# Optimization experiments

Hardware: AMD Instinct MI355X
Metric: run time of the kernel (lower is better)

The kernel has to match this reference:

```python
import jax, jax.numpy as jnp
import numpy as np

TGT, SRC, BH, D = 2048, 2048, 16, 64

def setup_inputs() -> dict:
    key = jax.random.key(0)
    kq, kk, kv, km = jax.random.split(key, 4)
    return {
        "query": jax.random.normal(kq, (TGT, BH, D), dtype=jnp.float32),
        "key": jax.random.normal(kk, (SRC, BH, D), dtype=jnp.float32),
        "value": jax.random.normal(kv, (SRC, BH, D), dtype=jnp.float32),
        "attn_mask": jax.random.randint(km, (1, TGT, SRC), 0, 2).astype(jnp.bool_),
    }

def reference(query, key, value, attn_mask):
    # seq-first layout: [len, batch_heads, head_dim] -> [bh, len, d]
    head_dim = query.shape[-1]
    q = jnp.swapaxes(query, 0, 1) * (float(head_dim) ** -0.5)  # [bh, tgt, d]
    k = jnp.swapaxes(key, 0, 1)                                # [bh, src, d]
    v = jnp.swapaxes(value, 0, 1)                              # [bh, src, d]
    w = jnp.einsum('btd,bsd->bts', q, k)                       # [bh, tgt, src]
    w = jnp.where(attn_mask, jnp.float32(-1e8), w)
    w = jax.nn.softmax(w, axis=-1)
    # dropout p=0.0 (eval) -> identity
    out = jnp.einsum('bts,bsd->btd', w, v)                     # [bh, tgt, d]
    return jnp.swapaxes(out, 0, 1), w  # ([tgt, bh, d], [bh, tgt, src])
```

## Files before the change

kernel.cpp:

```cpp
#include <hip/hip_runtime.h>

#define TGT 2048
#define SRC 2048
#define BH 16
#define HD 64
#define BT 16
#define SROW 2056

typedef __bf16 bf16x8 __attribute__((ext_vector_type(8)));
typedef unsigned short ushortx8 __attribute__((ext_vector_type(8)));
typedef float floatx4 __attribute__((ext_vector_type(4)));

__device__ int g_mask_is_u8;

__device__ __forceinline__ unsigned short f2bf(float f) {
  unsigned u = __builtin_bit_cast(unsigned, f);
  u += 0x7FFFu + ((u >> 16) & 1u);
  return (unsigned short)(u >> 16);
}
__device__ __forceinline__ float bf2f(unsigned short s) {
  unsigned u = ((unsigned)s) << 16;
  return __builtin_bit_cast(float, u);
}

__global__ void detect_mask_fmt(const unsigned char* __restrict__ m) {
  __shared__ int any;
  if (threadIdx.x == 0) any = 0;
  __syncthreads();
  int local = 0;
  int base = threadIdx.x * 16;
#pragma unroll
  for (int i = 0; i < 16; ++i) {
    int idx = base + i;
    if (idx & 3) local |= m[idx];
  }
  if (local) atomicOr(&any, 1);
  __syncthreads();
  if (threadIdx.x == 0) g_mask_is_u8 = (any != 0);
}

__global__ void mask_pack(const unsigned char* __restrict__ m8,
                          const int* __restrict__ m32,
                          unsigned char* __restrict__ bm) {
  const int gid = blockIdx.x * 256 + threadIdx.x;
  const bool is_u8 = (g_mask_is_u8 != 0);
  const size_t base = (size_t)gid * 32;
  unsigned bits = 0;
  if (is_u8) {
    const uint4 a = *(const uint4*)(m8 + base);
    const uint4 b = *(const uint4*)(m8 + base + 16);
    unsigned w[8] = {a.x, a.y, a.z, a.w, b.x, b.y, b.z, b.w};
#pragma unroll
    for (int wi = 0; wi < 8; ++wi)
#pragma unroll
      for (int j = 0; j < 4; ++j)
        if ((w[wi] >> (8 * j)) & 0xFFu) bits |= 1u << (wi * 4 + j);
  } else {
#pragma unroll
    for (int c = 0; c < 8; ++c) {
      const int4 a = *(const int4*)(m32 + base + c * 4);
      if (a.x) bits |= 1u << (c * 4 + 0);
      if (a.y) bits |= 1u << (c * 4 + 1);
      if (a.z) bits |= 1u << (c * 4 + 2);
      if (a.w) bits |= 1u << (c * 4 + 3);
    }
  }
  *(unsigned*)(bm + (size_t)gid * 4) = bits;
}

__global__ void cvt_qk(const float* __restrict__ q, const float* __restrict__ k,
                       unsigned short* __restrict__ qb, unsigned short* __restrict__ kb) {
  const int gid = blockIdx.x * 256 + threadIdx.x;
  const int half = TGT * BH * HD / 8;
  const float* src; unsigned short* dst; float sc;
  int idx;
  if (gid < half) { src = q; dst = qb; sc = 0.125f; idx = gid; }
  else            { src = k; dst = kb; sc = 1.0f;  idx = gid - half; }
  const float* p = src + (size_t)idx * 8;
  float4 a = *(const float4*)p;
  float4 b = *(const float4*)(p + 4);
  union { unsigned short u[8]; ushortx8 v; } o;
  o.u[0] = f2bf(a.x * sc); o.u[1] = f2bf(a.y * sc);
  o.u[2] = f2bf(a.z * sc); o.u[3] = f2bf(a.w * sc);
  o.u[4] = f2bf(b.x * sc); o.u[5] = f2bf(b.y * sc);
  o.u[6] = f2bf(b.z * sc); o.u[7] = f2bf(b.w * sc);
  *(ushortx8*)(dst + (size_t)idx * 8) = o.v;
}

__global__ void v_tr(const float* __restrict__ v, unsigned short* __restrict__ vt) {
  __shared__ unsigned short tile[64 * 72];
  const int h = blockIdx.x >> 5;
  const int s0 = (blockIdx.x & 31) * 64;
  const int tid = threadIdx.x;
  const int sr = tid >> 4, c = tid & 15;
#pragma unroll
  for (int p = 0; p < 4; ++p) {
    const int s = sr + p * 16;
    float4 f = *(const float4*)(v + (size_t)(s0 + s) * (BH * HD) + h * HD + c * 4);
    tile[(c * 4 + 0) * 72 + s] = f2bf(f.x);
    tile[(c * 4 + 1) * 72 + s] = f2bf(f.y);
    tile[(c * 4 + 2) * 72 + s] = f2bf(f.z);
    tile[(c * 4 + 3) * 72 + s] = f2bf(f.w);
  }
  __syncthreads();
  const int d = tid >> 2, q4 = tid & 3;
  ushortx8 o0 = *(const ushortx8*)&tile[d * 72 + q4 * 16];
  ushortx8 o1 = *(const ushortx8*)&tile[d * 72 + q4 * 16 + 8];
  unsigned short* dst = vt + (size_t)h * HD * SRC + (size_t)d * SRC + s0 + q4 * 16;
  *(ushortx8*)dst = o0;
  *(ushortx8*)(dst + 8) = o1;
}

__launch_bounds__(1024, 8)
__global__ void attn_kernel(const unsigned short* __restrict__ qb,
                            const unsigned short* __restrict__ kb,
                            const unsigned short* __restrict__ vtb,
                            const unsigned char* __restrict__ bmask,
                            float* __restrict__ out0,
                            float* __restrict__ wout) {
  extern __shared__ char smem[];
  unsigned short* smS = (unsigned short*)smem;
  float* scratch = (float*)(smem + BT * SROW * 2);
  float* maxpart = scratch + 3072;
  float* rowmaxArr = maxpart + 256;
  float* invArr = rowmaxArr + BT;

  const int bid0 = blockIdx.x;
  const int bid = (bid0 & 7) * 256 + (bid0 >> 3);
  const int h = bid >> 7;
  const int t0 = (bid & 127) * BT;
  const int tid = threadIdx.x;
  const int wv = tid >> 6;
  const int lane = tid & 63;
  const int quad = lane >> 4;
  const int l16 = lane & 15;

  {
    const unsigned* bg = (const unsigned*)(bmask + (size_t)t0 * (SRC / 8));
    ((unsigned*)scratch)[tid] = bg[tid];
  }

  bf16x8 aq[2];
  {
    const unsigned short* qp = qb + (size_t)(t0 + l16) * (BH * HD) + h * HD + quad * 8;
    aq[0] = __builtin_bit_cast(bf16x8, *(const ushortx8*)qp);
    aq[1] = __builtin_bit_cast(bf16x8, *(const ushortx8*)(qp + 32));
  }
  __syncthreads();

  const unsigned short* smBits = (const unsigned short*)scratch;
  float pmax[4] = {-3.4e38f, -3.4e38f, -3.4e38f, -3.4e38f};
  for (int st = wv; st < SRC / 16; st += 16) {
    const int sbase = st * 16;
    const unsigned short* kp = kb + (size_t)(sbase + l16) * (BH * HD) + h * HD + quad * 8;
    bf16x8 bk0 = __builtin_bit_cast(bf16x8, *(const ushortx8*)kp);
    bf16x8 bk1 = __builtin_bit_cast(bf16x8, *(const ushortx8*)(kp + 32));
    floatx4 c = {0.f, 0.f, 0.f, 0.f};
    c = __builtin_amdgcn_mfma_f32_16x16x32_bf16(aq[0], bk0, c, 0, 0, 0);
    c = __builtin_amdgcn_mfma_f32_16x16x32_bf16(aq[1], bk1, c, 0, 0, 0);
    const int scol = sbase + l16;
#pragma unroll
    for (int r = 0; r < 4; ++r) {
      const int tl = quad * 4 + r;
      const unsigned bits = smBits[tl * (SRC / 16) + st];
      const float val = ((bits >> l16) & 1u) ? -1e8f : c[r];
      pmax[r] = fmaxf(pmax[r], val);
      const float oth = __shfl_xor(val, 1);
      if (!(l16 & 1)) {
        unsigned pk2 = (unsigned)f2bf(val) | ((unsigned)f2bf(oth) << 16);
        *(unsigned*)&smS[tl * SROW + scol] = pk2;
      }
    }
  }
#pragma unroll
  for (int r = 0; r < 4; ++r) {
    float m = pmax[r];
    m = fmaxf(m, __shfl_xor(m, 1));
    m = fmaxf(m, __shfl_xor(m, 2));
    m = fmaxf(m, __shfl_xor(m, 4));
    m = fmaxf(m, __shfl_xor(m, 8));
    if (l16 == 0) maxpart[(quad * 4 + r) * 16 + wv] = m;
  }
  __syncthreads();
  if (tid < BT) {
    float m = maxpart[tid * 16];
    for (int j = 1; j < 16; ++j) m = fmaxf(m, maxpart[tid * 16 + j]);
    rowmaxArr[tid] = m;
  }
  __syncthreads();

  {
    const int row = tid >> 6;
    const int cc = tid & 63;
    const float rm = rowmaxArr[row];
    unsigned short* srow = smS + row * SROW;
    float psum = 0.f;
#pragma unroll
    for (int kk = 0; kk < 4; ++kk) {
      const int col = cc * 8 + kk * 512;
      ushortx8 u = *(const ushortx8*)&srow[col];
      union { unsigned short u[8]; ushortx8 v; } o;
#pragma unroll
      for (int i = 0; i < 8; ++i) {
        float e = __expf(bf2f(u[i]) - rm);
        psum += e;
        o.u[i] = f2bf(e);
      }
      *(ushortx8*)&srow[col] = o.v;
    }
    scratch[row * 64 + cc] = psum;
  }
  __syncthreads();
  if (tid < BT) {
    float s = 0.f;
    for (int j = 0; j < 64; ++j) s += scratch[tid * 64 + j];
    invArr[tid] = 1.0f / s;
  }
  __syncthreads();

  {
    const int row = tid >> 6;
    const int cc = tid & 63;
    const float invv = invArr[row];
    float* wrow = wout + ((size_t)h * TGT + (t0 + row)) * SRC;
    const unsigned short* srow = smS + row * SROW;
#pragma unroll
    for (int kk = 0; kk < 4; ++kk) {
      const int col = cc * 8 + kk * 512;
      ushortx8 u = *(const ushortx8*)&srow[col];
      float4 a, b;
      a.x = bf2f(u[0]) * invv; a.y = bf2f(u[1]) * invv;
      a.z = bf2f(u[2]) * invv; a.w = bf2f(u[3]) * invv;
      b.x = bf2f(u[4]) * invv; b.y = bf2f(u[5]) * invv;
      b.z = bf2f(u[6]) * invv; b.w = bf2f(u[7]) * invv;
      *(float4*)&wrow[col] = a;
      *(float4*)&wrow[col + 4] = b;
    }
  }

  {
    const int dt = wv & 3;
    const int qr = wv >> 2;
    const int dbase = dt * 16;
    const int sstart = qr * 512;
    const unsigned short* vp = vtb + (size_t)h * HD * SRC +
                               (size_t)(dbase + l16) * SRC + sstart + quad * 8;
    const unsigned short* sp = smS + l16 * SROW + sstart + quad * 8;
    floatx4 acc = {0.f, 0.f, 0.f, 0.f};
    for (int s0 = 0; s0 < 512; s0 += 32) {
      bf16x8 af = __builtin_bit_cast(bf16x8, *(const ushortx8*)(sp + s0));
      bf16x8 bfv = __builtin_bit_cast(bf16x8, *(const ushortx8*)(vp + s0));
      acc = __builtin_amdgcn_mfma_f32_16x16x32_bf16(af, bfv, acc, 0, 0, 0);
    }
    if (qr) {
#pragma unroll
      for (int r = 0; r < 4; ++r)
        scratch[((qr - 1) * 4 + dt) * 256 + (quad * 4 + r) * 16 + l16] = acc[r];
    }
    __syncthreads();
    if (!qr) {
#pragma unroll
      for (int r = 0; r < 4; ++r) {
        const int tl = quad * 4 + r;
        float s = acc[r] + scratch[(0 * 4 + dt) * 256 + tl * 16 + l16]
                         + scratch[(1 * 4 + dt) * 256 + tl * 16 + l16]
                         + scratch[(2 * 4 + dt) * 256 + tl * 16 + l16];
        out0[((size_t)(t0 + tl) * BH + h) * HD + dbase + l16] = s * invArr[tl];
      }
    }
  }
}

extern "C" void kernel_launch(void* const* d_in, const int* in_sizes, int n_in,
                              void* d_out, int out_size, void* d_ws, size_t ws_size,
                              hipStream_t stream) {
  const float* q = (const float*)d_in[0];
  const float* k = (const float*)d_in[1];
  const float* v = (const float*)d_in[2];
  const unsigned char* m8 = (const unsigned char*)d_in[3];
  const int* m32 = (const int*)d_in[3];
  float* out0 = (float*)d_out;
  float* wout = out0 + (size_t)TGT * BH * HD;

  unsigned short* qb = (unsigned short*)d_ws;
  unsigned short* kb = qb + (size_t)TGT * BH * HD;
  unsigned short* vt = kb + (size_t)SRC * BH * HD;
  unsigned char* bmask = (unsigned char*)(vt + (size_t)BH * HD * SRC);

  const size_t shbytes = (size_t)BT * SROW * 2 + 3072 * 4 + 256 * 4 + BT * 4 + BT * 4;
  hipFuncSetAttribute((const void*)attn_kernel,
                      hipFuncAttributeMaxDynamicSharedMemorySize, (int)shbytes);

  detect_mask_fmt<<<1, 256, 0, stream>>>(m8);
  mask_pack<<<dim3(512), dim3(256), 0, stream>>>(m8, m32, bmask);
  cvt_qk<<<dim3(2048), dim3(256), 0, stream>>>(q, k, qb, kb);
  v_tr<<<dim3(BH * (SRC / 64)), dim3(256), 0, stream>>>(v, vt);
  attn_kernel<<<dim3(BH * (TGT / BT)), dim3(1024), shbytes, stream>>>(
      qb, kb, vt, bmask, out0, wout);
}
```

Before: 433.3 us.

## Keep softmax scores in registers and fuse max, exp, normalize and store

The QK^T MFMA operands are swapped so each lane holds a row's scores for a contiguous chunk of columns. Each wave now handles a contiguous 128-column slice and keeps the masked scores in registers. Row max, exp, sum and normalisation run in registers with shuffle-plus-LDS reductions, and the weights are written straight to global memory and to LDS once for the PV MFMA. This removes the repeated LDS round-trips and several barriers of the separate softmax passes. It also pads the mask scratch rows and adds s_setprio around the MFMAs, at the cost of more registers per thread.

```diff
diff --git a/kernel.cpp b/kernel.cpp
--- a/kernel.cpp
+++ b/kernel.cpp
@@ -120,10 +120,11 @@
                             float* __restrict__ wout) {
   extern __shared__ char smem[];
   unsigned short* smS = (unsigned short*)smem;
-  float* scratch = (float*)(smem + BT * SROW * 2);
-  float* maxpart = scratch + 3072;
-  float* rowmaxArr = maxpart + 256;
-  float* invArr = rowmaxArr + BT;
+  float* dscratch = (float*)(smem + BT * SROW * 2);
+  unsigned* scratchM = (unsigned*)dscratch;
+  float* maxpart = dscratch + 1088;
+  float* sumpart = dscratch + 1344;
+  float* invArr = (float*)(smem + BT * SROW * 2 + 12288);
 
   const int bid0 = blockIdx.x;
   const int bid = (bid0 & 7) * 256 + (bid0 >> 3);
@@ -137,7 +138,8 @@
 
   {
     const unsigned* bg = (const unsigned*)(bmask + (size_t)t0 * (SRC / 8));
-    ((unsigned*)scratch)[tid] = bg[tid];
+    const int row = tid >> 6, col = tid & 63;
+    scratchM[row * 68 + col] = bg[row * 64 + col];
   }
 
   bf16x8 aq[2];
@@ -148,95 +150,89 @@
   }
   __syncthreads();
 
-  const unsigned short* smBits = (const unsigned short*)scratch;
-  float pmax[4] = {-3.4e38f, -3.4e38f, -3.4e38f, -3.4e38f};
-  for (int st = wv; st < SRC / 16; st += 16) {
-    const int sbase = st * 16;
+  const uint4 mw = *(const uint4*)&scratchM[l16 * 68 + wv * 4];
+
+  const int sb0 = wv * 128;
+  unsigned pp[16];
+  float pmax = -3.4e38f;
+#pragma unroll
+  for (int j = 0; j < 8; ++j) {
+    const int sbase = sb0 + j * 16;
     const unsigned short* kp = kb + (size_t)(sbase + l16) * (BH * HD) + h * HD + quad * 8;
     bf16x8 bk0 = __builtin_bit_cast(bf16x8, *(const ushortx8*)kp);
     bf16x8 bk1 = __builtin_bit_cast(bf16x8, *(const ushortx8*)(kp + 32));
     floatx4 c = {0.f, 0.f, 0.f, 0.f};
-    c = __builtin_amdgcn_mfma_f32_16x16x32_bf16(aq[0], bk0, c, 0, 0, 0);
-    c = __builtin_amdgcn_mfma_f32_16x16x32_bf16(aq[1], bk1, c, 0, 0, 0);
-    const int scol = sbase + l16;
-#pragma unroll
-    for (int r = 0; r < 4; ++r) {
-      const int tl = quad * 4 + r;
-      const unsigned bits = smBits[tl * (SRC / 16) + st];
-      const float val = ((bits >> l16) & 1u) ? -1e8f : c[r];
-      pmax[r] = fmaxf(pmax[r], val);
-      const float oth = __shfl_xor(val, 1);
-      if (!(l16 & 1)) {
-        unsigned pk2 = (unsigned)f2bf(val) | ((unsigned)f2bf(oth) << 16);
-        *(unsigned*)&smS[tl * SROW + scol] = pk2;
-      }
-    }
-  }
-#pragma unroll
-  for (int r = 0; r < 4; ++r) {
-    float m = pmax[r];
-    m = fmaxf(m, __shfl_xor(m, 1));
-    m = fmaxf(m, __shfl_xor(m, 2));
-    m = fmaxf(m, __shfl_xor(m, 4));
-    m = fmaxf(m, __shfl_xor(m, 8));
-    if (l16 == 0) maxpart[(quad * 4 + r) * 16 + wv] = m;
-  }
-  __syncthreads();
-  if (tid < BT) {
-    float m = maxpart[tid * 16];
-    for (int j = 1; j < 16; ++j) m = fmaxf(m, maxpart[tid * 16 + j]);
-    rowmaxArr[tid] = m;
-  }
-  __syncthreads();
-
-  {
-    const int row = tid >> 6;
-    const int cc = tid & 63;
-    const float rm = rowmaxArr[row];
-    unsigned short* srow = smS + row * SROW;
-    float psum = 0.f;
-#pragma unroll
-    for (int kk = 0; kk < 4; ++kk) {
-      const int col = cc * 8 + kk * 512;
-      ushortx8 u = *(const ushortx8*)&srow[col];
-      union { unsigned short u[8]; ushortx8 v; } o;
-#pragma unroll
-      for (int i = 0; i < 8; ++i) {
-        float e = __expf(bf2f(u[i]) - rm);
-        psum += e;
-        o.u[i] = f2bf(e);
-      }
-      *(ushortx8*)&srow[col] = o.v;
-    }
-    scratch[row * 64 + cc] = psum;
-  }
-  __syncthreads();
-  if (tid < BT) {
-    float s = 0.f;
-    for (int j = 0; j < 64; ++j) s += scratch[tid * 64 + j];
-    invArr[tid] = 1.0f / s;
-  }
-  __syncthreads();
-
-  {
-    const int row = tid >> 6;
-    const int cc = tid & 63;
-    const float invv = invArr[row];
-    float* wrow = wout + ((size_t)h * TGT + (t0 + row)) * SRC;
-    const unsigned short* srow = smS + row * SROW;
-#pragma unroll
-    for (int kk = 0; kk < 4; ++kk) {
-      const int col = cc * 8 + kk * 512;
-      ushortx8 u = *(const ushortx8*)&srow[col];
-      float4 a, b;
-      a.x = bf2f(u[0]) * invv; a.y = bf2f(u[1]) * invv;
-      a.z = bf2f(u[2]) * invv; a.w = bf2f(u[3]) * invv;
-      b.x = bf2f(u[4]) * invv; b.y = bf2f(u[5]) * invv;
-      b.z = bf2f(u[6]) * invv; b.w = bf2f(u[7]) * invv;
-      *(float4*)&wrow[col] = a;
-      *(float4*)&wrow[col + 4] = b;
-    }
-  }
+    __builtin_amdgcn_s_setprio(1);
+    c = __builtin_amdgcn_mfma_f32_16x16x32_bf16(bk0, aq[0], c, 0, 0, 0);
+    c = __builtin_amdgcn_mfma_f32_16x16x32_bf16(bk1, aq[1], c, 0, 0, 0);
+    __builtin_amdgcn_s_setprio(0);
+    const unsigned mword = (j < 2) ? mw.x : (j < 4) ? mw.y : (j < 6) ? mw.z : mw.w;
+    float v0, v1, v2, v3;
+    {
+      const int sh = ((j & 1) << 4) + (quad << 2);
+      v0 = ((mword >> (sh + 0)) & 1u) ? -1e8f : c[0];
+      v1 = ((mword >> (sh + 1)) & 1u) ? -1e8f : c[1];
+      v2 = ((mword >> (sh + 2)) & 1u) ? -1e8f : c[2];
+      v3 = ((mword >> (sh + 3)) & 1u) ? -1e8f : c[3];
+    }
+    pmax = fmaxf(pmax, fmaxf(fmaxf(v0, v1), fmaxf(v2, v3)));
+    pp[j * 2 + 0] = (unsigned)f2bf(v0) | ((unsigned)f2bf(v1) << 16);
+    pp[j * 2 + 1] = (unsigned)f2bf(v2) | ((unsigned)f2bf(v3) << 16);
+  }
+  pmax = fmaxf(pmax, __shfl_xor(pmax, 16));
+  pmax = fmaxf(pmax, __shfl_xor(pmax, 32));
+  if (lane < 16) maxpart[l16 * 16 + wv] = pmax;
+  __syncthreads();
+
+  float rm;
+  {
+    float4 m4 = *(const float4*)&maxpart[l16 * 16 + quad * 4];
+    rm = fmaxf(fmaxf(m4.x, m4.y), fmaxf(m4.z, m4.w));
+    rm = fmaxf(rm, __shfl_xor(rm, 16));
+    rm = fmaxf(rm, __shfl_xor(rm, 32));
+  }
+
+  float psum = 0.f;
+#pragma unroll
+  for (int j = 0; j < 16; ++j) {
+    const unsigned w2 = pp[j];
+    float e0 = __expf(bf2f((unsigned short)(w2 & 0xFFFF)) - rm);
+    float e1 = __expf(bf2f((unsigned short)(w2 >> 16)) - rm);
+    psum += e0 + e1;
+    pp[j] = (unsigned)f2bf(e0) | ((unsigned)f2bf(e1) << 16);
+  }
+  psum += __shfl_xor(psum, 16);
+  psum += __shfl_xor(psum, 32);
+  if (lane < 16) sumpart[l16 * 16 + wv] = psum;
+  __syncthreads();
+
+  float inv;
+  {
+    float4 s4 = *(const float4*)&sumpart[l16 * 16 + quad * 4];
+    float rs = (s4.x + s4.y) + (s4.z + s4.w);
+    rs += __shfl_xor(rs, 16);
+    rs += __shfl_xor(rs, 32);
+    inv = 1.0f / rs;
+  }
+  if (tid < BT) invArr[tid] = inv;
+
+  {
+    float* wrow = wout + ((size_t)h * TGT + (t0 + l16)) * SRC + sb0;
+    unsigned short* srow = smS + l16 * SROW + sb0;
+#pragma unroll
+    for (int j = 0; j < 8; ++j) {
+      const unsigned wa = pp[j * 2 + 0], wb = pp[j * 2 + 1];
+      float4 w4;
+      w4.x = bf2f((unsigned short)(wa & 0xFFFF)) * inv;
+      w4.y = bf2f((unsigned short)(wa >> 16)) * inv;
+      w4.z = bf2f((unsigned short)(wb & 0xFFFF)) * inv;
+      w4.w = bf2f((unsigned short)(wb >> 16)) * inv;
+      *(float4*)&wrow[j * 16 + quad * 4] = w4;
+      *(unsigned*)&srow[j * 16 + quad * 4] = wa;
+      *(unsigned*)&srow[j * 16 + quad * 4 + 2] = wb;
+    }
+  }
+  __syncthreads();
 
   {
     const int dt = wv & 3;
@@ -247,24 +243,26 @@
                                (size_t)(dbase + l16) * SRC + sstart + quad * 8;
     const unsigned short* sp = smS + l16 * SROW + sstart + quad * 8;
     floatx4 acc = {0.f, 0.f, 0.f, 0.f};
+    __builtin_amdgcn_s_setprio(1);
     for (int s0 = 0; s0 < 512; s0 += 32) {
       bf16x8 af = __builtin_bit_cast(bf16x8, *(const ushortx8*)(sp + s0));
       bf16x8 bfv = __builtin_bit_cast(bf16x8, *(const ushortx8*)(vp + s0));
       acc = __builtin_amdgcn_mfma_f32_16x16x32_bf16(af, bfv, acc, 0, 0, 0);
     }
+    __builtin_amdgcn_s_setprio(0);
     if (qr) {
 #pragma unroll
       for (int r = 0; r < 4; ++r)
-        scratch[((qr - 1) * 4 + dt) * 256 + (quad * 4 + r) * 16 + l16] = acc[r];
+        dscratch[((qr - 1) * 4 + dt) * 256 + (quad * 4 + r) * 16 + l16] = acc[r];
     }
     __syncthreads();
     if (!qr) {
 #pragma unroll
       for (int r = 0; r < 4; ++r) {
         const int tl = quad * 4 + r;
-        float s = acc[r] + scratch[(0 * 4 + dt) * 256 + tl * 16 + l16]
-                         + scratch[(1 * 4 + dt) * 256 + tl * 16 + l16]
-                         + scratch[(2 * 4 + dt) * 256 + tl * 16 + l16];
+        float s = acc[r] + dscratch[(0 * 4 + dt) * 256 + tl * 16 + l16]
+                         + dscratch[(1 * 4 + dt) * 256 + tl * 16 + l16]
+                         + dscratch[(2 * 4 + dt) * 256 + tl * 16 + l16];
         out0[((size_t)(t0 + tl) * BH + h) * HD + dbase + l16] = s * invArr[tl];
       }
     }
@@ -287,7 +285,7 @@
   unsigned short* vt = kb + (size_t)SRC * BH * HD;
   unsigned char* bmask = (unsigned char*)(vt + (size_t)BH * HD * SRC);
 
-  const size_t shbytes = (size_t)BT * SROW * 2 + 3072 * 4 + 256 * 4 + BT * 4 + BT * 4;
+  const size_t shbytes = (size_t)BT * SROW * 2 + 12288 + 64;
   hipFuncSetAttribute((const void*)attn_kernel,
                       hipFuncAttributeMaxDynamicSharedMemorySize, (int)shbytes);
 
```

Result: no change. 430.8 us (-0.6%).
